# Performance work log

Hardware: AMD Instinct MI355X
Metric: run time of the kernel (lower is better)

Reference implementation:

```python
import jax, jax.numpy as jnp
import numpy as np

N = 100000   # nodes
E = 600000   # edges
K = 3        # TAGConv hops
EPS = 1e-5   # BatchNorm eps
SLOPE = 0.01 # LeakyReLU negative slope


def setup_inputs() -> dict:
    key = jax.random.key(0)
    ks = jax.random.split(key, 8)
    y = jax.random.normal(ks[0], (N, 128), dtype=jnp.float32)
    edge_index = jax.random.randint(ks[1], (2, E), 0, N, dtype=jnp.int64)
    edge_attr = jax.random.uniform(ks[2], (E,), dtype=jnp.float32)
    # TAGConv layer l has (K+1) weight matrices [in, out]; bias only on first two layers
    W1 = 0.1 * jax.random.normal(ks[3], (K + 1, 128, 128), dtype=jnp.float32)
    b1 = jnp.full((128,), 0.1, dtype=jnp.float32)
    W2 = 0.1 * jax.random.normal(ks[4], (K + 1, 128, 128), dtype=jnp.float32)
    b2 = jnp.full((128,), 0.1, dtype=jnp.float32)
    W3 = 0.1 * jax.random.normal(ks[5], (K + 1, 128, 64), dtype=jnp.float32)
    g1 = jnp.ones((128,), jnp.float32); be1 = jnp.zeros((128,), jnp.float32)
    g2 = jnp.ones((128,), jnp.float32); be2 = jnp.zeros((128,), jnp.float32)
    g3 = jnp.ones((64,), jnp.float32);  be3 = jnp.zeros((64,), jnp.float32)
    return dict(y=y, edge_index=edge_index, edge_attr=edge_attr,
                W1=W1, b1=b1, g1=g1, be1=be1,
                W2=W2, b2=b2, g2=g2, be2=be2,
                W3=W3, g3=g3, be3=be3)


def _tag_conv(x, W, b, src, dst, norm):
    # out = sum_{k=0..K} A_hat^k x @ W_k (+ b)
    out = x @ W[0]
    h = x
    for k in range(1, W.shape[0]):
        h = jax.ops.segment_sum(norm[:, None] * h[src], dst, num_segments=N)
        out = out + h @ W[k]
    return out if b is None else out + b


def _bn(x, g, b):
    # BatchNorm1d training mode: biased batch stats over nodes
    m = x.mean(axis=0)
    v = jnp.mean((x - m) ** 2, axis=0)
    return (x - m) * jax.lax.rsqrt(v + EPS) * g + b


def reference(y, edge_index, edge_attr, W1, b1, g1, be1, W2, b2, g2, be2, W3, g3, be3):
    src, dst = edge_index[0], edge_index[1]
    # gcn_norm (symmetric, no self-loops): D^{-1/2} A D^{-1/2}
    deg = jax.ops.segment_sum(edge_attr, dst, num_segments=N)
    dis = jnp.where(deg > 0, jax.lax.rsqrt(jnp.maximum(deg, 1e-12)), 0.0)
    norm = dis[src] * edge_attr * dis[dst]
    lrelu = lambda t: jax.nn.leaky_relu(t, SLOPE)
    x = lrelu(_bn(_tag_conv(y, W1, b1, src, dst, norm), g1, be1))
    x = lrelu(_bn(_tag_conv(x, W2, b2, src, dst, norm), g2, be2))
    x = lrelu(_bn(_tag_conv(x, W3, None, src, dst, norm), g3, be3))
    return x
```

## Files before the change

kernel.cpp:

```cpp
#include <hip/hip_runtime.h>
#include <hip/hip_bf16.h>

typedef unsigned short b16;
typedef __attribute__((ext_vector_type(8))) unsigned short us8;
typedef __attribute__((ext_vector_type(8))) short short8;
typedef __attribute__((ext_vector_type(4))) float float4v;

#define NN 100000
#define NE 600000

__device__ __forceinline__ float bf2f(b16 u) {
    return __uint_as_float(((unsigned)u) << 16);
}
__device__ __forceinline__ b16 f2bf(float f) {
    unsigned x = __float_as_uint(f);
    return (b16)((x + 0x7fffu + ((x >> 16) & 1u)) >> 16);
}

__global__ void k_detect(const void* __restrict__ y, const void* __restrict__ ei,
                         int* __restrict__ flags) {
    if (threadIdx.x == 0 && blockIdx.x == 0) {
        const b16* p = (const b16*)y;
        int f32 = 0;
        for (int i = 0; i < 128; ++i) {
            float v = bf2f(p[i]);
            if (!(fabsf(v) < 1e4f)) { f32 = 1; break; }
        }
        flags[0] = f32;
        const long long* q = (const long long*)ei;
        int i64 = 1;
        for (int i = 0; i < 4; ++i) {
            long long v = q[i];
            if (v < 0 || v >= NN) i64 = 0;
        }
        flags[1] = i64;
    }
}

__global__ void k_cvt(const void* __restrict__ in, float* __restrict__ out, int n,
                      const int* __restrict__ flags) {
    int i = blockIdx.x * blockDim.x + threadIdx.x;
    if (i >= n) return;
    out[i] = flags[0] ? ((const float*)in)[i] : bf2f(((const b16*)in)[i]);
}

__global__ void k_idx(const void* __restrict__ ei, int* __restrict__ src32,
                      int* __restrict__ dst32, const int* __restrict__ flags) {
    int e = blockIdx.x * blockDim.x + threadIdx.x;
    if (e >= NE) return;
    int s, d;
    if (flags[1]) {
        const long long* p = (const long long*)ei;
        s = (int)p[e];
        d = (int)p[NE + e];
    } else {
        const int* p = (const int*)ei;
        s = p[e];
        d = p[NE + e];
    }
    src32[e] = ((unsigned)s < NN) ? s : 0;
    dst32[e] = ((unsigned)d < NN) ? d : 0;
}

__global__ void k_degcnt(const int* __restrict__ dst, const void* __restrict__ ea,
                         float* __restrict__ deg, int* __restrict__ cnt,
                         const int* __restrict__ flags) {
    int e = blockIdx.x * blockDim.x + threadIdx.x;
    if (e >= NE) return;
    float w = flags[0] ? ((const float*)ea)[e] : bf2f(((const b16*)ea)[e]);
    int d = dst[e];
    unsafeAtomicAdd(&deg[d], w);
    atomicAdd(&cnt[d], 1);
}

__global__ void k_dis(float* deg) {
    int n = blockIdx.x * blockDim.x + threadIdx.x;
    if (n < NN) {
        float d = deg[n];
        deg[n] = (d > 0.f) ? rsqrtf(fmaxf(d, 1e-12f)) : 0.f;
    }
}

#define SCAN_B 1024
#define SCAN_NB ((NN + SCAN_B - 1) / SCAN_B)

__global__ __launch_bounds__(SCAN_B) void k_scan1(const int* __restrict__ cnt,
                                                  int* __restrict__ inc,
                                                  int* __restrict__ bsum) {
    __shared__ int s[SCAN_B];
    int i = blockIdx.x * SCAN_B + threadIdx.x;
    s[threadIdx.x] = (i < NN) ? cnt[i] : 0;
    __syncthreads();
    for (int off = 1; off < SCAN_B; off <<= 1) {
        int t = (threadIdx.x >= off) ? s[threadIdx.x - off] : 0;
        __syncthreads();
        s[threadIdx.x] += t;
        __syncthreads();
    }
    if (i < NN) inc[i] = s[threadIdx.x];
    if (threadIdx.x == SCAN_B - 1) bsum[blockIdx.x] = s[SCAN_B - 1];
}

__global__ void k_scan2(int* bsum) {
    if (threadIdx.x == 0 && blockIdx.x == 0) {
        int a = 0;
        for (int i = 0; i < SCAN_NB; ++i) {
            int t = bsum[i];
            bsum[i] = a;
            a += t;
        }
    }
}

__global__ void k_scan3(const int* __restrict__ inc, const int* __restrict__ bsum,
                        int* __restrict__ rowptr) {
    int i = blockIdx.x * blockDim.x + threadIdx.x;
    if (i == 0) rowptr[0] = 0;
    if (i < NN) rowptr[i + 1] = inc[i] + bsum[i / SCAN_B];
}

__global__ void k_fill(const int* __restrict__ src, const int* __restrict__ dst,
                       const void* __restrict__ ea, const float* __restrict__ dis,
                       const int* __restrict__ rowptr, int* __restrict__ fill,
                       int* __restrict__ csrc, float* __restrict__ cw,
                       const int* __restrict__ flags) {
    int e = blockIdx.x * blockDim.x + threadIdx.x;
    if (e >= NE) return;
    float a = flags[0] ? ((const float*)ea)[e] : bf2f(((const b16*)ea)[e]);
    int d = dst[e];
    int s = src[e];
    int pos = rowptr[d] + atomicAdd(&fill[d], 1);
    csrc[pos] = s;
    cw[pos] = dis[s] * a * dis[d];
}

__global__ void k_pack(const void* __restrict__ W, b16* __restrict__ Wp, int NC,
                       const int* __restrict__ flags) {
    int f = blockIdx.x * blockDim.x + threadIdx.x;
    int total = 512 * NC / 8;
    if (f >= total) return;
    int lane = f & 63;
    int rest = f >> 6;
    int CT = NC >> 4;
    int ct = rest % CT, ks = rest / CT;
    int k0 = 32 * ks + (lane >> 4) * 8;
    int col = 16 * ct + (lane & 15);
    us8 v;
#pragma unroll
    for (int j = 0; j < 8; ++j) {
        float x = flags[0] ? ((const float*)W)[(size_t)(k0 + j) * NC + col]
                           : bf2f(((const b16*)W)[(size_t)(k0 + j) * NC + col]);
        v[j] = f2bf(x);
    }
    *(us8*)&Wp[(size_t)f * 8] = v;
}

__global__ void k_cast(const void* __restrict__ y, b16* __restrict__ XC,
                       const int* __restrict__ flags) {
    int i = blockIdx.x * blockDim.x + threadIdx.x;
    if (i >= NN * 32) return;
    int row = i >> 5, cg = i & 31;
    float4 v;
    if (flags[0]) {
        v = ((const float4*)y)[i];
    } else {
        ushort4 u = ((const ushort4*)y)[i];
        v = make_float4(bf2f(u.x), bf2f(u.y), bf2f(u.z), bf2f(u.w));
    }
    ushort4 o;
    o.x = f2bf(v.x); o.y = f2bf(v.y); o.z = f2bf(v.z); o.w = f2bf(v.w);
    *(ushort4*)&XC[(size_t)row * 512 + 4 * cg] = o;
}

__global__ __launch_bounds__(256) void k_spmm(b16* __restrict__ XC, int ci, int co,
                                              const int* __restrict__ rowptr,
                                              const int* __restrict__ csrc,
                                              const float* __restrict__ cw) {
    int gid = blockIdx.x * blockDim.x + threadIdx.x;
    int node = gid >> 6;
    if (node >= NN) return;
    int lane = gid & 63;
    int half = lane >> 5;
    int l31 = lane & 31;
    int beg = rowptr[node], end = rowptr[node + 1];

    float4 a0 = make_float4(0.f, 0.f, 0.f, 0.f);
    float4 a1 = make_float4(0.f, 0.f, 0.f, 0.f);
    int i = beg;
    for (; i + 3 < end; i += 4) {
        int e0 = i + half, e1 = i + 2 + half;
        int s0 = csrc[e0];
        float w0 = cw[e0];
        int s1 = csrc[e1];
        float w1 = cw[e1];
        ushort4 u0 = *(const ushort4*)&XC[(size_t)s0 * 512 + ci + 4 * l31];
        ushort4 u1 = *(const ushort4*)&XC[(size_t)s1 * 512 + ci + 4 * l31];
        a0.x = fmaf(w0, bf2f(u0.x), a0.x);
        a0.y = fmaf(w0, bf2f(u0.y), a0.y);
        a0.z = fmaf(w0, bf2f(u0.z), a0.z);
        a0.w = fmaf(w0, bf2f(u0.w), a0.w);
        a1.x = fmaf(w1, bf2f(u1.x), a1.x);
        a1.y = fmaf(w1, bf2f(u1.y), a1.y);
        a1.z = fmaf(w1, bf2f(u1.z), a1.z);
        a1.w = fmaf(w1, bf2f(u1.w), a1.w);
    }
    for (; i < end; i += 2) {
        bool act = (half == 0) || (i + 1 < end);
        int ee = act ? (i + half) : i;
        float w = act ? cw[ee] : 0.f;
        int s = csrc[ee];
        ushort4 u = *(const ushort4*)&XC[(size_t)s * 512 + ci + 4 * l31];
        a0.x = fmaf(w, bf2f(u.x), a0.x);
        a0.y = fmaf(w, bf2f(u.y), a0.y);
        a0.z = fmaf(w, bf2f(u.z), a0.z);
        a0.w = fmaf(w, bf2f(u.w), a0.w);
    }
    a0.x += a1.x;
    a0.y += a1.y;
    a0.z += a1.z;
    a0.w += a1.w;
    a0.x += __shfl_xor(a0.x, 32);
    a0.y += __shfl_xor(a0.y, 32);
    a0.z += __shfl_xor(a0.z, 32);
    a0.w += __shfl_xor(a0.w, 32);
    if (half == 0) {
        ushort4 o;
        o.x = f2bf(a0.x);
        o.y = f2bf(a0.y);
        o.z = f2bf(a0.z);
        o.w = f2bf(a0.w);
        *(ushort4*)&XC[(size_t)node * 512 + co + 4 * l31] = o;
    }
}

template <int NC>
__global__ __launch_bounds__(256) void k_mgemm(const b16* __restrict__ XC,
                                               const b16* __restrict__ Wp,
                                               const float* __restrict__ bias,
                                               float* __restrict__ OUT,
                                               float* __restrict__ gsum,
                                               float* __restrict__ gsq) {
    constexpr int CT = NC / 16;
    __shared__ b16 As[128 * 40];
    __shared__ b16 Bs[CT * 512];
    __shared__ float csum[NC], csq[NC];
    const int tid = threadIdx.x;
    const int wave = tid >> 6;
    const int lane = tid & 63;
    const int row0 = blockIdx.x * 128;
    const int quad = lane >> 4;
    const int l15 = lane & 15;

    float4v acc[2][CT];
#pragma unroll
    for (int rt = 0; rt < 2; ++rt)
#pragma unroll
        for (int ct = 0; ct < CT; ++ct) acc[rt][ct] = (float4v)(0.f);
    for (int i = tid; i < NC; i += 256) {
        csum[i] = 0.f;
        csq[i] = 0.f;
    }

    const int arow = tid >> 1;
    const int apart = tid & 1;
    int grow = row0 + arow;
    if (grow >= NN) grow = NN - 1;
    const b16* gA = XC + (size_t)grow * 512 + apart * 16;
    b16* lA = As + arow * 40 + apart * 16;

    for (int ks = 0; ks < 16; ++ks) {
        us8 a0 = *(const us8*)(gA + 32 * ks);
        us8 a1 = *(const us8*)(gA + 32 * ks + 8);
        *(us8*)lA = a0;
        *(us8*)(lA + 8) = a1;
        const us8* gB = (const us8*)(Wp + (size_t)ks * CT * 512);
#pragma unroll
        for (int q = 0; q < CT * 64 / 256; ++q)
            ((us8*)Bs)[q * 256 + tid] = gB[q * 256 + tid];
        __syncthreads();

        short8 af[2], bf[CT];
#pragma unroll
        for (int rt = 0; rt < 2; ++rt)
            af[rt] = *(const short8*)&As[(32 * wave + 16 * rt + l15) * 40 + quad * 8];
#pragma unroll
        for (int ct = 0; ct < CT; ++ct)
            bf[ct] = *(const short8*)&Bs[ct * 512 + lane * 8];
#pragma unroll
        for (int rt = 0; rt < 2; ++rt)
#pragma unroll
            for (int ct = 0; ct < CT; ++ct)
                acc[rt][ct] = __builtin_amdgcn_mfma_f32_16x16x32_bf16(
                    af[rt], bf[ct], acc[rt][ct], 0, 0, 0);
        __syncthreads();
    }

#pragma unroll
    for (int rt = 0; rt < 2; ++rt) {
#pragma unroll
        for (int ct = 0; ct < CT; ++ct) {
            int col = 16 * ct + l15;
            float bv = bias ? bias[col] : 0.f;
            float s = 0.f, sq = 0.f;
#pragma unroll
            for (int r = 0; r < 4; ++r) {
                int row = row0 + 32 * wave + 16 * rt + quad * 4 + r;
                if (row < NN) {
                    float v = acc[rt][ct][r] + bv;
                    OUT[(size_t)row * NC + col] = v;
                    s += v;
                    sq += v * v;
                }
            }
            s += __shfl_xor(s, 16);
            s += __shfl_xor(s, 32);
            sq += __shfl_xor(sq, 16);
            sq += __shfl_xor(sq, 32);
            if (quad == 0) {
                atomicAdd(&csum[col], s);
                atomicAdd(&csq[col], sq);
            }
        }
    }
    __syncthreads();
    for (int i = tid; i < NC; i += 256) {
        unsafeAtomicAdd(&gsum[i], csum[i]);
        unsafeAtomicAdd(&gsq[i], csq[i]);
    }
}

__global__ void k_bnparam(const float* gsum, const float* gsq, const float* g,
                          const float* be, float* scale, float* shift, int ncols) {
    int c = threadIdx.x;
    if (c < ncols) {
        float m = gsum[c] * (1.f / NN);
        float v = gsq[c] * (1.f / NN) - m * m;
        v = fmaxf(v, 0.f);
        float s = rsqrtf(v + 1e-5f) * g[c];
        scale[c] = s;
        shift[c] = be[c] - m * s;
    }
}

__global__ void k_bnapply_mid(const float* __restrict__ OUT,
                              const float* __restrict__ scale,
                              const float* __restrict__ shift, b16* __restrict__ XC) {
    int i = blockIdx.x * blockDim.x + threadIdx.x;
    if (i >= NN * 64) return;
    int row = i >> 6, c = (i & 63) * 2;
    float2 v = *(const float2*)&OUT[(size_t)row * 128 + c];
    float a = fmaf(v.x, scale[c], shift[c]);
    float b = fmaf(v.y, scale[c + 1], shift[c + 1]);
    a = a > 0.f ? a : 0.01f * a;
    b = b > 0.f ? b : 0.01f * b;
    ushort2 o;
    o.x = f2bf(a);
    o.y = f2bf(b);
    *(ushort2*)&XC[(size_t)row * 512 + c] = o;
}

__global__ void k_bnapply_last(const float* __restrict__ OUT,
                               const float* __restrict__ scale,
                               const float* __restrict__ shift, void* __restrict__ dout,
                               const int* __restrict__ flags) {
    int i = blockIdx.x * blockDim.x + threadIdx.x;
    if (i >= NN * 64) return;
    int c = i & 63;
    float v = fmaf(OUT[i], scale[c], shift[c]);
    v = v > 0.f ? v : 0.01f * v;
    if (flags[0])
        ((float*)dout)[i] = v;
    else
        ((b16*)dout)[i] = f2bf(v);
}

#define PB_B1 0
#define PB_B2 128
#define PB_G1 256
#define PB_BE1 384
#define PB_G2 512
#define PB_BE2 640
#define PB_G3 768
#define PB_BE3 832
#define PB_SZ 896

extern "C" void kernel_launch(void* const* d_in, const int* in_sizes, int n_in,
                              void* d_out, int out_size, void* d_ws, size_t ws_size,
                              hipStream_t stream) {
    const void* y   = d_in[0];
    const void* ei  = d_in[1];
    const void* ea  = d_in[2];
    const void* W1  = d_in[3];
    const void* b1  = d_in[4];
    const void* g1  = d_in[5];
    const void* be1 = d_in[6];
    const void* W2  = d_in[7];
    const void* b2  = d_in[8];
    const void* g2  = d_in[9];
    const void* be2 = d_in[10];
    const void* W3  = d_in[11];
    const void* g3  = d_in[12];
    const void* be3 = d_in[13];

    char* w = (char*)d_ws;
    size_t used = 0;
    auto carve = [&](size_t bytes) -> char* {
        char* p = w + used;
        used += (bytes + 255) & ~(size_t)255;
        return p;
    };

    int* flags   = (int*)carve(16);
    int* src32   = (int*)carve((size_t)NE * 4);
    int* dst32   = (int*)carve((size_t)NE * 4);
    float* deg   = (float*)carve((size_t)NN * 4);
    int* cnt     = (int*)carve((size_t)NN * 4);
    int* rowptr  = (int*)carve((size_t)(NN + 1) * 4);
    int* cscan   = (int*)carve((size_t)NN * 4);
    int* bsum    = (int*)carve((size_t)SCAN_NB * 4);
    int* csrc    = (int*)carve((size_t)NE * 4);
    float* cw    = (float*)carve((size_t)NE * 4);
    float* PB    = (float*)carve(PB_SZ * 4);
    b16* Wp1     = (b16*)carve((size_t)512 * 128 * 2);
    b16* Wp2     = (b16*)carve((size_t)512 * 128 * 2);
    b16* Wp3     = (b16*)carve((size_t)512 * 64 * 2);
    float* OUT   = (float*)carve((size_t)NN * 128 * 4);
    float* gsum  = (float*)carve(128 * 4);
    float* gsq   = (float*)carve(128 * 4);
    float* scale = (float*)carve(128 * 4);
    float* shift = (float*)carve(128 * 4);
    b16* XC      = (b16*)carve((size_t)NN * 512 * 2);

    k_detect<<<1, 64, 0, stream>>>(y, ei, flags);
    auto cvt = [&](const void* in, float* out, int n) {
        k_cvt<<<(n + 127) / 128, 128, 0, stream>>>(in, out, n, flags);
    };
    cvt(b1, PB + PB_B1, 128);
    cvt(b2, PB + PB_B2, 128);
    cvt(g1, PB + PB_G1, 128);
    cvt(be1, PB + PB_BE1, 128);
    cvt(g2, PB + PB_G2, 128);
    cvt(be2, PB + PB_BE2, 128);
    cvt(g3, PB + PB_G3, 64);
    cvt(be3, PB + PB_BE3, 64);
    k_pack<<<(512 * 128 / 8 + 255) / 256, 256, 0, stream>>>(W1, Wp1, 128, flags);
    k_pack<<<(512 * 128 / 8 + 255) / 256, 256, 0, stream>>>(W2, Wp2, 128, flags);
    k_pack<<<(512 * 64 / 8 + 255) / 256, 256, 0, stream>>>(W3, Wp3, 64, flags);

    k_idx<<<(NE + 255) / 256, 256, 0, stream>>>(ei, src32, dst32, flags);
    hipMemsetAsync(deg, 0, (size_t)NN * 4, stream);
    hipMemsetAsync(cnt, 0, (size_t)NN * 4, stream);
    k_degcnt<<<(NE + 255) / 256, 256, 0, stream>>>(dst32, ea, deg, cnt, flags);
    k_dis<<<(NN + 255) / 256, 256, 0, stream>>>(deg);
    k_scan1<<<SCAN_NB, SCAN_B, 0, stream>>>(cnt, cscan, bsum);
    k_scan2<<<1, 64, 0, stream>>>(bsum);
    k_scan3<<<(NN + 255) / 256, 256, 0, stream>>>(cscan, bsum, rowptr);
    hipMemsetAsync(cnt, 0, (size_t)NN * 4, stream);
    k_fill<<<(NE + 255) / 256, 256, 0, stream>>>(src32, dst32, ea, deg, rowptr, cnt,
                                                 csrc, cw, flags);

    k_cast<<<(NN * 32 + 255) / 256, 256, 0, stream>>>(y, XC, flags);

    auto spmm = [&](int ci, int co) {
        k_spmm<<<(NN * 64 + 255) / 256, 256, 0, stream>>>(XC, ci, co, rowptr, csrc, cw);
    };
    const int gemm_grid = (NN + 127) / 128;

    auto layer = [&](const b16* Wp, const float* bias, const float* g, const float* be,
                     int NC, bool last) {
        spmm(0, 128);
        spmm(128, 256);
        spmm(256, 384);
        hipMemsetAsync(gsum, 0, NC * 4, stream);
        hipMemsetAsync(gsq, 0, NC * 4, stream);
        if (NC == 128)
            k_mgemm<128><<<gemm_grid, 256, 0, stream>>>(XC, Wp, bias, OUT, gsum, gsq);
        else
            k_mgemm<64><<<gemm_grid, 256, 0, stream>>>(XC, Wp, bias, OUT, gsum, gsq);
        k_bnparam<<<1, NC, 0, stream>>>(gsum, gsq, g, be, scale, shift, NC);
        if (last)
            k_bnapply_last<<<(NN * 64 + 255) / 256, 256, 0, stream>>>(OUT, scale, shift,
                                                                      d_out, flags);
        else
            k_bnapply_mid<<<(NN * 64 + 255) / 256, 256, 0, stream>>>(OUT, scale, shift,
                                                                     XC);
    };

    layer(Wp1, PB + PB_B1, PB + PB_G1, PB + PB_BE1, 128, false);
    layer(Wp2, PB + PB_B2, PB + PB_G2, PB + PB_BE2, 128, false);
    layer(Wp3, nullptr, PB + PB_G3, PB + PB_BE3, 64, true);
}
```

Measured before the change: 835.6 us.

## Widen SpMM gathers, double-buffer GEMM tiles, store pre-BN output in bf16

After: 800.8 us. -4.2%, faster.

```diff
diff --git a/kernel.cpp b/kernel.cpp
--- a/kernel.cpp
+++ b/kernel.cpp
@@ -180,56 +180,52 @@
     int node = gid >> 6;
     if (node >= NN) return;
     int lane = gid & 63;
-    int half = lane >> 5;
-    int l31 = lane & 31;
+    int grp = lane >> 4;
+    int l15 = lane & 15;
     int beg = rowptr[node], end = rowptr[node + 1];
 
-    float4 a0 = make_float4(0.f, 0.f, 0.f, 0.f);
-    float4 a1 = make_float4(0.f, 0.f, 0.f, 0.f);
+    float a0[8], a1[8];
+#pragma unroll
+    for (int j = 0; j < 8; ++j) {
+        a0[j] = 0.f;
+        a1[j] = 0.f;
+    }
     int i = beg;
-    for (; i + 3 < end; i += 4) {
-        int e0 = i + half, e1 = i + 2 + half;
+    for (; i + 7 < end; i += 8) {
+        int e0 = i + grp, e1 = i + 4 + grp;
         int s0 = csrc[e0];
         float w0 = cw[e0];
         int s1 = csrc[e1];
         float w1 = cw[e1];
-        ushort4 u0 = *(const ushort4*)&XC[(size_t)s0 * 512 + ci + 4 * l31];
-        ushort4 u1 = *(const ushort4*)&XC[(size_t)s1 * 512 + ci + 4 * l31];
-        a0.x = fmaf(w0, bf2f(u0.x), a0.x);
-        a0.y = fmaf(w0, bf2f(u0.y), a0.y);
-        a0.z = fmaf(w0, bf2f(u0.z), a0.z);
-        a0.w = fmaf(w0, bf2f(u0.w), a0.w);
-        a1.x = fmaf(w1, bf2f(u1.x), a1.x);
-        a1.y = fmaf(w1, bf2f(u1.y), a1.y);
-        a1.z = fmaf(w1, bf2f(u1.z), a1.z);
-        a1.w = fmaf(w1, bf2f(u1.w), a1.w);
-    }
-    for (; i < end; i += 2) {
-        bool act = (half == 0) || (i + 1 < end);
-        int ee = act ? (i + half) : i;
+        us8 u0 = *(const us8*)&XC[(size_t)s0 * 512 + ci + 8 * l15];
+        us8 u1 = *(const us8*)&XC[(size_t)s1 * 512 + ci + 8 * l15];
+#pragma unroll
+        for (int j = 0; j < 8; ++j) {
+            a0[j] = fmaf(w0, bf2f(u0[j]), a0[j]);
+            a1[j] = fmaf(w1, bf2f(u1[j]), a1[j]);
+        }
+    }
+    for (; i < end; i += 4) {
+        int e = i + grp;
+        bool act = e < end;
+        int ee = act ? e : (end - 1);
         float w = act ? cw[ee] : 0.f;
         int s = csrc[ee];
-        ushort4 u = *(const ushort4*)&XC[(size_t)s * 512 + ci + 4 * l31];
-        a0.x = fmaf(w, bf2f(u.x), a0.x);
-        a0.y = fmaf(w, bf2f(u.y), a0.y);
-        a0.z = fmaf(w, bf2f(u.z), a0.z);
-        a0.w = fmaf(w, bf2f(u.w), a0.w);
-    }
-    a0.x += a1.x;
-    a0.y += a1.y;
-    a0.z += a1.z;
-    a0.w += a1.w;
-    a0.x += __shfl_xor(a0.x, 32);
-    a0.y += __shfl_xor(a0.y, 32);
-    a0.z += __shfl_xor(a0.z, 32);
-    a0.w += __shfl_xor(a0.w, 32);
-    if (half == 0) {
-        ushort4 o;
-        o.x = f2bf(a0.x);
-        o.y = f2bf(a0.y);
-        o.z = f2bf(a0.z);
-        o.w = f2bf(a0.w);
-        *(ushort4*)&XC[(size_t)node * 512 + co + 4 * l31] = o;
+        us8 u = *(const us8*)&XC[(size_t)s * 512 + ci + 8 * l15];
+#pragma unroll
+        for (int j = 0; j < 8; ++j) a0[j] = fmaf(w, bf2f(u[j]), a0[j]);
+    }
+#pragma unroll
+    for (int j = 0; j < 8; ++j) a0[j] += a1[j];
+#pragma unroll
+    for (int j = 0; j < 8; ++j) a0[j] += __shfl_xor(a0[j], 16);
+#pragma unroll
+    for (int j = 0; j < 8; ++j) a0[j] += __shfl_xor(a0[j], 32);
+    if (grp == 0) {
+        us8 o;
+#pragma unroll
+        for (int j = 0; j < 8; ++j) o[j] = f2bf(a0[j]);
+        *(us8*)&XC[(size_t)node * 512 + co + 8 * l15] = o;
     }
 }
 
@@ -237,89 +233,84 @@
 __global__ __launch_bounds__(256) void k_mgemm(const b16* __restrict__ XC,
                                                const b16* __restrict__ Wp,
                                                const float* __restrict__ bias,
-                                               float* __restrict__ OUT,
+                                               b16* __restrict__ OUT,
                                                float* __restrict__ gsum,
                                                float* __restrict__ gsq) {
     constexpr int CT = NC / 16;
-    __shared__ b16 As[128 * 40];
-    __shared__ b16 Bs[CT * 512];
+    __shared__ b16 As[2][64 * 40];
+    __shared__ b16 Bs[2][CT * 512];
     __shared__ float csum[NC], csq[NC];
     const int tid = threadIdx.x;
     const int wave = tid >> 6;
     const int lane = tid & 63;
-    const int row0 = blockIdx.x * 128;
+    const int row0 = blockIdx.x * 64;
     const int quad = lane >> 4;
     const int l15 = lane & 15;
 
-    float4v acc[2][CT];
-#pragma unroll
-    for (int rt = 0; rt < 2; ++rt)
-#pragma unroll
-        for (int ct = 0; ct < CT; ++ct) acc[rt][ct] = (float4v)(0.f);
+    float4v acc[CT];
+#pragma unroll
+    for (int ct = 0; ct < CT; ++ct) acc[ct] = (float4v)(0.f);
     for (int i = tid; i < NC; i += 256) {
         csum[i] = 0.f;
         csq[i] = 0.f;
     }
 
-    const int arow = tid >> 1;
-    const int apart = tid & 1;
+    const int arow = tid >> 2;
+    const int apart = tid & 3;
     int grow = row0 + arow;
     if (grow >= NN) grow = NN - 1;
-    const b16* gA = XC + (size_t)grow * 512 + apart * 16;
-    b16* lA = As + arow * 40 + apart * 16;
+    const b16* gA = XC + (size_t)grow * 512 + apart * 8;
+    b16* lA0 = &As[0][arow * 40 + apart * 8];
+    b16* lA1 = &As[1][arow * 40 + apart * 8];
+
+    *(us8*)lA0 = *(const us8*)gA;
+    {
+        const us8* gB = (const us8*)Wp;
+#pragma unroll
+        for (int q = 0; q < CT * 64 / 256; ++q)
+            ((us8*)Bs[0])[q * 256 + tid] = gB[q * 256 + tid];
+    }
 
     for (int ks = 0; ks < 16; ++ks) {
-        us8 a0 = *(const us8*)(gA + 32 * ks);
-        us8 a1 = *(const us8*)(gA + 32 * ks + 8);
-        *(us8*)lA = a0;
-        *(us8*)(lA + 8) = a1;
-        const us8* gB = (const us8*)(Wp + (size_t)ks * CT * 512);
-#pragma unroll
-        for (int q = 0; q < CT * 64 / 256; ++q)
-            ((us8*)Bs)[q * 256 + tid] = gB[q * 256 + tid];
+        int buf = ks & 1;
         __syncthreads();
-
-        short8 af[2], bf[CT];
-#pragma unroll
-        for (int rt = 0; rt < 2; ++rt)
-            af[rt] = *(const short8*)&As[(32 * wave + 16 * rt + l15) * 40 + quad * 8];
-#pragma unroll
-        for (int ct = 0; ct < CT; ++ct)
-            bf[ct] = *(const short8*)&Bs[ct * 512 + lane * 8];
-#pragma unroll
-        for (int rt = 0; rt < 2; ++rt)
-#pragma unroll
-            for (int ct = 0; ct < CT; ++ct)
-                acc[rt][ct] = __builtin_amdgcn_mfma_f32_16x16x32_bf16(
-                    af[rt], bf[ct], acc[rt][ct], 0, 0, 0);
-        __syncthreads();
-    }
-
-#pragma unroll
-    for (int rt = 0; rt < 2; ++rt) {
+        if (ks < 15) {
+            *(us8*)(buf ? lA0 : lA1) = *(const us8*)(gA + 32 * (ks + 1));
+            const us8* gB = (const us8*)(Wp + (size_t)(ks + 1) * CT * 512);
+#pragma unroll
+            for (int q = 0; q < CT * 64 / 256; ++q)
+                ((us8*)Bs[buf ^ 1])[q * 256 + tid] = gB[q * 256 + tid];
+        }
+        short8 af = *(const short8*)&As[buf][(wave * 16 + l15) * 40 + quad * 8];
 #pragma unroll
         for (int ct = 0; ct < CT; ++ct) {
-            int col = 16 * ct + l15;
-            float bv = bias ? bias[col] : 0.f;
-            float s = 0.f, sq = 0.f;
-#pragma unroll
-            for (int r = 0; r < 4; ++r) {
-                int row = row0 + 32 * wave + 16 * rt + quad * 4 + r;
-                if (row < NN) {
-                    float v = acc[rt][ct][r] + bv;
-                    OUT[(size_t)row * NC + col] = v;
-                    s += v;
-                    sq += v * v;
-                }
+            short8 bf = *(const short8*)&Bs[buf][ct * 512 + lane * 8];
+            acc[ct] = __builtin_amdgcn_mfma_f32_16x16x32_bf16(af, bf, acc[ct], 0, 0, 0);
+        }
+    }
+
+#pragma unroll
+    for (int ct = 0; ct < CT; ++ct) {
+        int col = 16 * ct + l15;
+        float bv = bias ? bias[col] : 0.f;
+        float s = 0.f, sq = 0.f;
+#pragma unroll
+        for (int r = 0; r < 4; ++r) {
+            int row = row0 + wave * 16 + quad * 4 + r;
+            if (row < NN) {
+                float v = acc[ct][r] + bv;
+                OUT[(size_t)row * NC + col] = f2bf(v);
+                s += v;
+                sq += v * v;
             }
-            s += __shfl_xor(s, 16);
-            s += __shfl_xor(s, 32);
-            sq += __shfl_xor(sq, 16);
-            sq += __shfl_xor(sq, 32);
-            if (quad == 0) {
-                atomicAdd(&csum[col], s);
-                atomicAdd(&csq[col], sq);
-            }
+        }
+        s += __shfl_xor(s, 16);
+        s += __shfl_xor(s, 32);
+        sq += __shfl_xor(sq, 16);
+        sq += __shfl_xor(sq, 32);
+        if (quad == 0) {
+            atomicAdd(&csum[col], s);
+            atomicAdd(&csq[col], sq);
         }
     }
     __syncthreads();
@@ -342,15 +333,15 @@
     }
 }
 
-__global__ void k_bnapply_mid(const float* __restrict__ OUT,
+__global__ void k_bnapply_mid(const b16* __restrict__ OUT,
                               const float* __restrict__ scale,
                               const float* __restrict__ shift, b16* __restrict__ XC) {
     int i = blockIdx.x * blockDim.x + threadIdx.x;
     if (i >= NN * 64) return;
     int row = i >> 6, c = (i & 63) * 2;
-    float2 v = *(const float2*)&OUT[(size_t)row * 128 + c];
-    float a = fmaf(v.x, scale[c], shift[c]);
-    float b = fmaf(v.y, scale[c + 1], shift[c + 1]);
+    ushort2 u = *(const ushort2*)&OUT[(size_t)row * 128 + c];
+    float a = fmaf(bf2f(u.x), scale[c], shift[c]);
+    float b = fmaf(bf2f(u.y), scale[c + 1], shift[c + 1]);
     a = a > 0.f ? a : 0.01f * a;
     b = b > 0.f ? b : 0.01f * b;
     ushort2 o;
@@ -359,14 +350,14 @@
     *(ushort2*)&XC[(size_t)row * 512 + c] = o;
 }
 
-__global__ void k_bnapply_last(const float* __restrict__ OUT,
+__global__ void k_bnapply_last(const b16* __restrict__ OUT,
                                const float* __restrict__ scale,
                                const float* __restrict__ shift, void* __restrict__ dout,
                                const int* __restrict__ flags) {
     int i = blockIdx.x * blockDim.x + threadIdx.x;
     if (i >= NN * 64) return;
     int c = i & 63;
-    float v = fmaf(OUT[i], scale[c], shift[c]);
+    float v = fmaf(bf2f(OUT[i]), scale[c], shift[c]);
     v = v > 0.f ? v : 0.01f * v;
     if (flags[0])
         ((float*)dout)[i] = v;
@@ -424,7 +415,7 @@
     b16* Wp1     = (b16*)carve((size_t)512 * 128 * 2);
     b16* Wp2     = (b16*)carve((size_t)512 * 128 * 2);
     b16* Wp3     = (b16*)carve((size_t)512 * 64 * 2);
-    float* OUT   = (float*)carve((size_t)NN * 128 * 4);
+    b16* OUT     = (b16*)carve((size_t)NN * 128 * 2);
     float* gsum  = (float*)carve(128 * 4);
     float* gsq   = (float*)carve(128 * 4);
     float* scale = (float*)carve(128 * 4);
@@ -464,7 +455,7 @@
     auto spmm = [&](int ci, int co) {
         k_spmm<<<(NN * 64 + 255) / 256, 256, 0, stream>>>(XC, ci, co, rowptr, csrc, cw);
     };
-    const int gemm_grid = (NN + 127) / 128;
+    const int gemm_grid = (NN + 63) / 64;
 
     auto layer = [&](const b16* Wp, const float* bias, const float* g, const float* be,
                      int NC, bool last) {
```
